# Optimization experiments

Measured on AMD Instinct MI355X. Metric: run time of the kernel, lower is better.

Reference implementation:

```python
import jax, jax.numpy as jnp
import numpy as np

DIM = 512
NUM_HEADS = 16
WIN = (7, 7)
SIZE = WIN[0] * WIN[1]  # 49
B = 2048   # total windows
NW = 4     # windows per image (mask groups)


def _relative_position_index():
    coords_h = np.arange(WIN[0])
    coords_w = np.arange(WIN[1])
    coords = np.stack(np.meshgrid(coords_h, coords_w, indexing='ij'))  # [2,Wh,Ww]
    flat = coords.reshape(2, -1)                                       # [2,S]
    rel = flat[:, :, None] - flat[:, None, :]                          # [2,S,S]
    rel = rel.transpose(1, 2, 0)                                       # [S,S,2]
    rel[:, :, 0] += WIN[0] - 1
    rel[:, :, 1] += WIN[1] - 1
    rel[:, :, 0] *= 2 * WIN[1] - 1
    return rel.sum(-1).astype(np.int32)                                # [S,S]


def setup_inputs() -> dict:
    key = jax.random.key(0)
    ks = jax.random.split(key, 8)
    num_bias = (2 * WIN[0] - 1) * (2 * WIN[1] - 1)  # 169
    sd = 1.0 / np.sqrt(DIM)
    return {
        'x': jax.random.normal(ks[0], (B, SIZE, DIM), dtype=jnp.float32),
        'mask': jax.random.normal(ks[1], (NW, SIZE, SIZE), dtype=jnp.float32),
        'w_qkv': jax.random.normal(ks[2], (DIM, 3 * DIM), dtype=jnp.float32) * sd,
        'b_qkv': jnp.zeros((3 * DIM,), dtype=jnp.float32),
        'w_proj': jax.random.normal(ks[3], (DIM, DIM), dtype=jnp.float32) * sd,
        'b_proj': jnp.zeros((DIM,), dtype=jnp.float32),
        'bias_table': jax.random.normal(ks[4], (num_bias, NUM_HEADS), dtype=jnp.float32) * 0.02,
        'rel_idx': jnp.asarray(_relative_position_index()),
    }


def reference(x, mask, w_qkv, b_qkv, w_proj, b_proj, bias_table, rel_idx):
    b, s, c = x.shape
    h = NUM_HEADS
    hd = c // h
    scale = hd ** (-0.5)
    # qkv projection -> [3, B, H, S, hd]
    qkv = (x @ w_qkv + b_qkv).reshape(b, s, 3, h, hd).transpose(2, 0, 3, 1, 4)
    q, k, v = qkv[0] * scale, qkv[1], qkv[2]
    attn = jnp.einsum('bhqd,bhkd->bhqk', q, k)                 # [B,H,S,S]
    # gathered relative position bias -> [H,S,S]
    bias = bias_table[rel_idx.reshape(-1)].reshape(s, s, h).transpose(2, 0, 1)
    attn = attn + bias[None]
    nw = mask.shape[0]
    attn = attn.reshape(b // nw, nw, h, s, s) + mask[None, :, None]
    attn = jax.nn.softmax(attn.reshape(b, h, s, s), axis=-1)
    out = jnp.einsum('bhqk,bhkd->bhqd', attn, v)               # [B,H,S,hd]
    out = out.transpose(0, 2, 1, 3).reshape(b, s, c)
    return out @ w_proj + b_proj
```

## Files before the change

### kernel.cpp

```cpp
#include <hip/hip_runtime.h>
#include <hip/hip_bf16.h>
#include <stdint.h>

typedef float  floatx4 __attribute__((ext_vector_type(4)));
typedef short  short8  __attribute__((ext_vector_type(8)));
typedef unsigned short u16;

#define DIM 512
#define NH 16
#define HD 32
#define WS 49
#define NBW 2048
#define NWIN 4
#define M_TOTAL (NBW*WS)
#define N_QKV (3*DIM)

__device__ __forceinline__ u16 f2bf(float f) {
    uint32_t u = __float_as_uint(f);
    u += 0x7FFFu + ((u >> 16) & 1u);
    return (u16)(u >> 16);
}

__device__ __forceinline__ void load_lds16(const u16* g, u16* l) {
    __builtin_amdgcn_global_load_lds(
        (const __attribute__((address_space(1))) unsigned int*)g,
        (__attribute__((address_space(3))) unsigned int*)l, 16, 0, 0);
}

__global__ void cast_x_kernel(const float* __restrict__ in, u16* __restrict__ out, int n4) {
    int i = blockIdx.x * blockDim.x + threadIdx.x;
    if (i >= n4) return;
    const float4 v = ((const float4*)in)[i];
    ushort4 o;
    o.x = f2bf(v.x); o.y = f2bf(v.y); o.z = f2bf(v.z); o.w = f2bf(v.w);
    ((ushort4*)out)[i] = o;
}

__global__ void transpose_cast_kernel(const float* __restrict__ in, u16* __restrict__ out,
                                      int N, int total) {
    int idx = blockIdx.x * blockDim.x + threadIdx.x;
    if (idx >= total) return;
    int k = idx & (DIM - 1);
    int n = idx >> 9;
    out[idx] = f2bf(in[k * N + n]);
}

__global__ void build_comb_kernel(const float* __restrict__ bias_table, const int* __restrict__ rel_idx,
                                  const float* __restrict__ mask, float* __restrict__ comb) {
    int idx = blockIdx.x * blockDim.x + threadIdx.x;
    if (idx >= NWIN * NH * 64 * 64) return;
    int c = idx & 3, jj = (idx >> 2) & 15, i = (idx >> 6) & 63, h = (idx >> 12) & 15, g = idx >> 16;
    int j = c * 16 + jj;
    float v = -1e30f;
    if (i < WS && j < WS)
        v = bias_table[rel_idx[i * WS + j] * NH + h] + mask[(g * WS + i) * WS + j];
    comb[idx] = v;
}

template<bool OUT_BF16>
__global__ __launch_bounds__(256, 2) void gemm_bt_kernel(
    const u16* __restrict__ A, const u16* __restrict__ Bt,
    const float* __restrict__ bias, void* __restrict__ out, int N, int K)
{
    __shared__ __align__(16) u16 sA[128 * 32];
    __shared__ __align__(16) u16 sB[128 * 32];
    const int tid  = threadIdx.x;
    const int lane = tid & 63;
    const int wave = tid >> 6;
    const long m0 = (long)blockIdx.y * 128;
    const long n0 = (long)blockIdx.x * 128;
    const int rr = lane & 15;
    const int qk = (lane >> 4) * 8;
    const int wm = (wave >> 1) * 64;
    const int wn = (wave & 1) * 64;

    floatx4 acc[4][4];
    const floatx4 z4 = {0.f, 0.f, 0.f, 0.f};
#pragma unroll
    for (int mi = 0; mi < 4; ++mi)
#pragma unroll
        for (int ni = 0; ni < 4; ++ni) acc[mi][ni] = z4;

    const int row0 = tid >> 2;
    const int kc0  = (tid & 3) * 8;
    const u16* gA0 = A  + (m0 + row0) * K + kc0;
    const u16* gA1 = A  + (m0 + row0 + 64) * K + kc0;
    const u16* gB0 = Bt + (n0 + row0) * K + kc0;
    const u16* gB1 = Bt + (n0 + row0 + 64) * K + kc0;
    u16* lA0 = sA + tid * 8;
    u16* lA1 = sA + (tid + 256) * 8;
    u16* lB0 = sB + tid * 8;
    u16* lB1 = sB + (tid + 256) * 8;

    for (int k0 = 0; k0 < K; k0 += 32) {
        load_lds16(gA0 + k0, lA0);
        load_lds16(gA1 + k0, lA1);
        load_lds16(gB0 + k0, lB0);
        load_lds16(gB1 + k0, lB1);
        __syncthreads();
        short8 af[4], bfr[4];
#pragma unroll
        for (int mi = 0; mi < 4; ++mi)
            af[mi] = *(const short8*)(sA + (wm + mi * 16 + rr) * 32 + qk);
#pragma unroll
        for (int ni = 0; ni < 4; ++ni)
            bfr[ni] = *(const short8*)(sB + (wn + ni * 16 + rr) * 32 + qk);
#pragma unroll
        for (int mi = 0; mi < 4; ++mi)
#pragma unroll
            for (int ni = 0; ni < 4; ++ni)
                acc[mi][ni] = __builtin_amdgcn_mfma_f32_16x16x32_bf16(af[mi], bfr[ni], acc[mi][ni], 0, 0, 0);
        __syncthreads();
    }

#pragma unroll
    for (int mi = 0; mi < 4; ++mi) {
#pragma unroll
        for (int r = 0; r < 4; ++r) {
            const long m = m0 + wm + mi * 16 + (lane >> 4) * 4 + r;
#pragma unroll
            for (int ni = 0; ni < 4; ++ni) {
                const long n = n0 + wn + ni * 16 + rr;
                float v = acc[mi][ni][r] + bias[n];
                if (OUT_BF16) ((u16*)out)[m * N + n] = f2bf(v);
                else          ((float*)out)[m * N + n] = v;
            }
        }
    }
}

__global__ __launch_bounds__(256, 4) void attn_kernel(
    const u16* __restrict__ qkv, const float* __restrict__ comb,
    u16* __restrict__ attn_out)
{
    const int w   = threadIdx.x >> 6;
    const int l   = threadIdx.x & 63;
    const int job = blockIdx.x * 4 + w;
    const int b    = job >> 5;
    const int h    = (job >> 1) & 15;
    const int half = job & 1;
    const int row0 = half * 32;
    const int rr = l & 15;
    const int q4 = l >> 4;
    const int qk = q4 * 8;

    __shared__ __align__(16) u16 p_s[4][32 * 64];
    u16* ps = p_s[w];

    const u16* qg = qkv + (long)b * WS * N_QKV + h * HD;
    const u16* kg = qg + DIM;
    const u16* vg = qg + 2 * DIM;

    const short8 z8 = {0, 0, 0, 0, 0, 0, 0, 0};
    const floatx4 z4 = {0.f, 0.f, 0.f, 0.f};

    short8 af[2], bfr[4];
#pragma unroll
    for (int mi = 0; mi < 2; ++mi) {
        const int row = row0 + mi * 16 + rr;
        af[mi] = (row < WS) ? *(const short8*)(qg + (long)row * N_QKV + qk) : z8;
    }
#pragma unroll
    for (int ni = 0; ni < 4; ++ni) {
        const int row = ni * 16 + rr;
        bfr[ni] = (row < WS) ? *(const short8*)(kg + (long)row * N_QKV + qk) : z8;
    }

    short8 vf[2][2];
#pragma unroll
    for (int kk = 0; kk < 2; ++kk)
#pragma unroll
        for (int ni = 0; ni < 2; ++ni) {
            short8 t = z8;
            const int d = 2 * rr + ni;
#pragma unroll
            for (int j = 0; j < 8; ++j) {
                const int s = kk * 32 + qk + j;
                if (s < WS) t[j] = (short)vg[(long)s * N_QKV + d];
            }
            vf[kk][ni] = t;
        }
    short8 vones;
#pragma unroll
    for (int j = 0; j < 8; ++j) vones[j] = (short)0x3F80;

    floatx4 sc[2][4];
#pragma unroll
    for (int mi = 0; mi < 2; ++mi)
#pragma unroll
        for (int ni = 0; ni < 4; ++ni)
            sc[mi][ni] = __builtin_amdgcn_mfma_f32_16x16x32_bf16(af[mi], bfr[ni], z4, 0, 0, 0);

    const float4* cb4 = (const float4*)comb + ((long)((b & (NWIN - 1)) * NH + h)) * 1024;
    const float scale = 0.17677669529663689f;
#pragma unroll
    for (int mi = 0; mi < 2; ++mi) {
#pragma unroll
        for (int r = 0; r < 4; ++r) {
            const int il = mi * 16 + q4 * 4 + r;
            const float4 cb = cb4[(row0 + il) * 16 + rr];
            float e0 = __expf(sc[mi][0][r] * scale + cb.x);
            float e1 = __expf(sc[mi][1][r] * scale + cb.y);
            float e2 = __expf(sc[mi][2][r] * scale + cb.z);
            float e3 = __expf(sc[mi][3][r] * scale + cb.w);
#pragma unroll
            for (int c = 0; c < 4; ++c) {
                const int col = c * 16 + rr;
                const int blk = (col >> 3) ^ (il & 7);
                const float ev = (c == 0) ? e0 : (c == 1) ? e1 : (c == 2) ? e2 : e3;
                ps[il * 64 + blk * 8 + (col & 7)] = f2bf(ev);
            }
        }
    }
    asm volatile("s_waitcnt lgkmcnt(0)" ::: "memory");

    floatx4 oacc[2][3];
#pragma unroll
    for (int mi = 0; mi < 2; ++mi) { oacc[mi][0] = z4; oacc[mi][1] = z4; oacc[mi][2] = z4; }
#pragma unroll
    for (int kk = 0; kk < 2; ++kk) {
        short8 pf[2];
#pragma unroll
        for (int mi = 0; mi < 2; ++mi) {
            const int i2 = mi * 16 + rr;
            pf[mi] = *(const short8*)(ps + i2 * 64 + (((4 * kk + q4) ^ (i2 & 7)) * 8));
        }
#pragma unroll
        for (int mi = 0; mi < 2; ++mi) {
            oacc[mi][0] = __builtin_amdgcn_mfma_f32_16x16x32_bf16(pf[mi], vf[kk][0], oacc[mi][0], 0, 0, 0);
            oacc[mi][1] = __builtin_amdgcn_mfma_f32_16x16x32_bf16(pf[mi], vf[kk][1], oacc[mi][1], 0, 0, 0);
            oacc[mi][2] = __builtin_amdgcn_mfma_f32_16x16x32_bf16(pf[mi], vones,     oacc[mi][2], 0, 0, 0);
        }
    }

#pragma unroll
    for (int mi = 0; mi < 2; ++mi) {
#pragma unroll
        for (int r = 0; r < 4; ++r) {
            const int ig = row0 + mi * 16 + q4 * 4 + r;
            if (ig < WS) {
                const float inv = 1.0f / oacc[mi][2][r];
                const uint32_t lo = f2bf(oacc[mi][0][r] * inv);
                const uint32_t hi = f2bf(oacc[mi][1][r] * inv);
                uint32_t* op = (uint32_t*)(attn_out + ((long)(b * WS + ig)) * DIM + h * HD);
                op[rr] = lo | (hi << 16);
            }
        }
    }
}

extern "C" void kernel_launch(void* const* d_in, const int* in_sizes, int n_in,
                              void* d_out, int out_size, void* d_ws, size_t ws_size,
                              hipStream_t stream)
{
    const float* x          = (const float*)d_in[0];
    const float* mask       = (const float*)d_in[1];
    const float* w_qkv      = (const float*)d_in[2];
    const float* b_qkv      = (const float*)d_in[3];
    const float* w_proj     = (const float*)d_in[4];
    const float* b_proj     = (const float*)d_in[5];
    const float* bias_table = (const float*)d_in[6];
    const int*   rel_idx    = (const int*)d_in[7];
    float* out = (float*)d_out;

    char* ws = (char*)d_ws;
    u16* x_bf   = (u16*)ws;  ws += (size_t)M_TOTAL * DIM * 2;
    u16* wqkvT  = (u16*)ws;  ws += (size_t)N_QKV * DIM * 2;
    u16* wprojT = (u16*)ws;  ws += (size_t)DIM * DIM * 2;
    float* comb = (float*)ws; ws += (size_t)NWIN * NH * 64 * 64 * 4;
    u16* qkv    = (u16*)ws;  ws += (size_t)M_TOTAL * N_QKV * 2;
    u16* attn_o = x_bf;

    const int n4 = M_TOTAL * DIM / 4;
    cast_x_kernel<<<(n4 + 255) / 256, 256, 0, stream>>>(x, x_bf, n4);
    transpose_cast_kernel<<<(N_QKV * DIM + 255) / 256, 256, 0, stream>>>(w_qkv, wqkvT, N_QKV, N_QKV * DIM);
    transpose_cast_kernel<<<(DIM * DIM + 255) / 256, 256, 0, stream>>>(w_proj, wprojT, DIM, DIM * DIM);
    build_comb_kernel<<<(NWIN * NH * 64 * 64 + 255) / 256, 256, 0, stream>>>(bias_table, rel_idx, mask, comb);

    gemm_bt_kernel<true><<<dim3(N_QKV / 128, M_TOTAL / 128), 256, 0, stream>>>(
        x_bf, wqkvT, b_qkv, qkv, N_QKV, DIM);

    attn_kernel<<<NBW * NH * 2 / 4, 256, 0, stream>>>(qkv, comb, attn_o);

    gemm_bt_kernel<false><<<dim3(DIM / 128, M_TOTAL / 128), 256, 0, stream>>>(
        attn_o, wprojT, b_proj, out, DIM, DIM);
}
```

Baseline: 856.7 us.

## Replace 128x128 GEMM with double-buffered 256x256 tile GEMM using XCD-aware block remap

Both projection GEMMs move to a 512-thread kernel with 256x256 output tiles and double-buffered LDS over 64-wide K steps. Global-to-LDS loads for the next stage are interleaved with MFMA phases, using explicit vmcnt waits, barriers and s_setprio. Blocks are remapped across the eight XCDs to improve L2 locality. This raises arithmetic intensity and overlaps memory with compute, at the cost of more registers (8x4 accumulators) and more LDS per block. M_TOTAL is 100352 = 392*256, so tiles divide evenly.

```diff
diff --git a/kernel.cpp b/kernel.cpp
--- a/kernel.cpp
+++ b/kernel.cpp
@@ -57,71 +57,134 @@
     comb[idx] = v;
 }
 
+#define STAGE_HALF(BASE, DST, Q, KH, KCOL)                                            \
+    do {                                                                              \
+        load_lds16((BASE) + (long)(s0 >> 2) * K + (KCOL) + (KH) * 32 + (s0 & 3) * 8,  \
+                   &DST[Q][KH][s0 * 8]);                                              \
+        load_lds16((BASE) + (long)(s1 >> 2) * K + (KCOL) + (KH) * 32 + (s1 & 3) * 8,  \
+                   &DST[Q][KH][s1 * 8]);                                              \
+    } while (0)
+
+#define LDA4(P, MG, KH)                                                               \
+    _Pragma("unroll")                                                                 \
+    for (int mi = 0; mi < 4; ++mi)                                                    \
+        af[mi] = *(const short8*)(&sA[P][KH][(wm + (MG) * 64 + mi * 16 + rr) * 32 + q4 * 8]);
+
+#define LDB4(P, KH)                                                                   \
+    _Pragma("unroll")                                                                 \
+    for (int ni = 0; ni < 4; ++ni)                                                    \
+        bf[ni] = *(const short8*)(&sB[P][KH][(wn + ni * 16 + rr) * 32 + q4 * 8]);
+
+#define MFMA16(MG)                                                                    \
+    _Pragma("unroll")                                                                 \
+    for (int mi = 0; mi < 4; ++mi)                                                    \
+        _Pragma("unroll")                                                             \
+        for (int ni = 0; ni < 4; ++ni)                                                \
+            acc[(MG) * 4 + mi][ni] = __builtin_amdgcn_mfma_f32_16x16x32_bf16(         \
+                af[mi], bf[ni], acc[(MG) * 4 + mi][ni], 0, 0, 0);
+
 template<bool OUT_BF16>
-__global__ __launch_bounds__(256, 2) void gemm_bt_kernel(
+__global__ __launch_bounds__(512, 2) void gemm256_kernel(
     const u16* __restrict__ A, const u16* __restrict__ Bt,
     const float* __restrict__ bias, void* __restrict__ out, int N, int K)
 {
-    __shared__ __align__(16) u16 sA[128 * 32];
-    __shared__ __align__(16) u16 sB[128 * 32];
+    __shared__ __align__(16) u16 sA[2][2][256 * 32];
+    __shared__ __align__(16) u16 sB[2][2][256 * 32];
+
     const int tid  = threadIdx.x;
     const int lane = tid & 63;
-    const int wave = tid >> 6;
-    const long m0 = (long)blockIdx.y * 128;
-    const long n0 = (long)blockIdx.x * 128;
-    const int rr = lane & 15;
-    const int qk = (lane >> 4) * 8;
-    const int wm = (wave >> 1) * 64;
-    const int wn = (wave & 1) * 64;
-
-    floatx4 acc[4][4];
+    const int w    = tid >> 6;
+    const int rr   = lane & 15;
+    const int q4   = lane >> 4;
+    const int wm   = (w >> 2) * 128;
+    const int wn   = (w & 3) * 64;
+
+    const int nwg = gridDim.x;
+    const int lid = (blockIdx.x & 7) * (nwg >> 3) + (blockIdx.x >> 3);
+    const int GX  = N >> 8;
+    const int bx  = lid % GX;
+    const int by  = lid / GX;
+    const long m0 = (long)by * 256;
+    const long n0 = (long)bx * 256;
+
+    const u16* Ab = A  + m0 * K;
+    const u16* Bb = Bt + n0 * K;
+
+    const int s0 = tid;
+    const int s1 = tid + 512;
+
+    floatx4 acc[8][4];
     const floatx4 z4 = {0.f, 0.f, 0.f, 0.f};
 #pragma unroll
-    for (int mi = 0; mi < 4; ++mi)
-#pragma unroll
-        for (int ni = 0; ni < 4; ++ni) acc[mi][ni] = z4;
-
-    const int row0 = tid >> 2;
-    const int kc0  = (tid & 3) * 8;
-    const u16* gA0 = A  + (m0 + row0) * K + kc0;
-    const u16* gA1 = A  + (m0 + row0 + 64) * K + kc0;
-    const u16* gB0 = Bt + (n0 + row0) * K + kc0;
-    const u16* gB1 = Bt + (n0 + row0 + 64) * K + kc0;
-    u16* lA0 = sA + tid * 8;
-    u16* lA1 = sA + (tid + 256) * 8;
-    u16* lB0 = sB + tid * 8;
-    u16* lB1 = sB + (tid + 256) * 8;
-
-    for (int k0 = 0; k0 < K; k0 += 32) {
-        load_lds16(gA0 + k0, lA0);
-        load_lds16(gA1 + k0, lA1);
-        load_lds16(gB0 + k0, lB0);
-        load_lds16(gB1 + k0, lB1);
-        __syncthreads();
-        short8 af[4], bfr[4];
-#pragma unroll
-        for (int mi = 0; mi < 4; ++mi)
-            af[mi] = *(const short8*)(sA + (wm + mi * 16 + rr) * 32 + qk);
-#pragma unroll
-        for (int ni = 0; ni < 4; ++ni)
-            bfr[ni] = *(const short8*)(sB + (wn + ni * 16 + rr) * 32 + qk);
-#pragma unroll
-        for (int mi = 0; mi < 4; ++mi)
-#pragma unroll
-            for (int ni = 0; ni < 4; ++ni)
-                acc[mi][ni] = __builtin_amdgcn_mfma_f32_16x16x32_bf16(af[mi], bfr[ni], acc[mi][ni], 0, 0, 0);
-        __syncthreads();
-    }
-
-#pragma unroll
-    for (int mi = 0; mi < 4; ++mi) {
-#pragma unroll
-        for (int r = 0; r < 4; ++r) {
-            const long m = m0 + wm + mi * 16 + (lane >> 4) * 4 + r;
-#pragma unroll
-            for (int ni = 0; ni < 4; ++ni) {
-                const long n = n0 + wn + ni * 16 + rr;
-                float v = acc[mi][ni][r] + bias[n];
+    for (int i = 0; i < 8; ++i)
+#pragma unroll
+        for (int j = 0; j < 4; ++j) acc[i][j] = z4;
+
+    const int nk = K >> 6;
+
+#pragma unroll
+    for (int kh = 0; kh < 2; ++kh) {
+        STAGE_HALF(Ab, sA, 0, kh, 0);
+        STAGE_HALF(Bb, sB, 0, kh, 0);
+    }
+    asm volatile("s_waitcnt vmcnt(4)" ::: "memory");
+    __builtin_amdgcn_s_barrier();
+
+    for (int it = 0; it < nk; ++it) {
+        const int  p  = it & 1, q = p ^ 1;
+        const int  kn = (it + 1) << 6;
+        const bool hn = (it + 1 < nk);
+        short8 af[4], bf[4];
+
+        if (hn) STAGE_HALF(Ab, sA, q, 0, kn);
+        LDB4(p, 0)
+        LDA4(p, 0, 0)
+        __builtin_amdgcn_s_barrier();
+        __builtin_amdgcn_s_setprio(1);
+        MFMA16(0)
+        __builtin_amdgcn_s_setprio(0);
+        __builtin_amdgcn_s_barrier();
+
+        if (hn) STAGE_HALF(Bb, sB, q, 0, kn);
+        LDA4(p, 1, 0)
+        __builtin_amdgcn_s_barrier();
+        __builtin_amdgcn_s_setprio(1);
+        MFMA16(1)
+        __builtin_amdgcn_s_setprio(0);
+        if (hn) { asm volatile("s_waitcnt vmcnt(4)" ::: "memory"); }
+        else    { asm volatile("s_waitcnt vmcnt(0)" ::: "memory"); }
+        __builtin_amdgcn_s_barrier();
+
+        if (hn) STAGE_HALF(Ab, sA, q, 1, kn);
+        LDB4(p, 1)
+        LDA4(p, 0, 1)
+        __builtin_amdgcn_s_barrier();
+        __builtin_amdgcn_s_setprio(1);
+        MFMA16(0)
+        __builtin_amdgcn_s_setprio(0);
+        __builtin_amdgcn_s_barrier();
+
+        if (hn) STAGE_HALF(Bb, sB, q, 1, kn);
+        LDA4(p, 1, 1)
+        __builtin_amdgcn_s_barrier();
+        __builtin_amdgcn_s_setprio(1);
+        MFMA16(1)
+        __builtin_amdgcn_s_setprio(0);
+        if (hn) { asm volatile("s_waitcnt vmcnt(4)" ::: "memory"); }
+        __builtin_amdgcn_s_barrier();
+    }
+
+#pragma unroll
+    for (int nf = 0; nf < 4; ++nf) {
+        const long n = n0 + wn + nf * 16 + rr;
+        const float bv = bias[n];
+#pragma unroll
+        for (int mf = 0; mf < 8; ++mf) {
+            const long mrow = m0 + wm + mf * 16 + q4 * 4;
+#pragma unroll
+            for (int r = 0; r < 4; ++r) {
+                const long m = mrow + r;
+                const float v = acc[mf][nf][r] + bv;
                 if (OUT_BF16) ((u16*)out)[m * N + n] = f2bf(v);
                 else          ((float*)out)[m * N + n] = v;
             }
@@ -277,11 +340,11 @@
     transpose_cast_kernel<<<(DIM * DIM + 255) / 256, 256, 0, stream>>>(w_proj, wprojT, DIM, DIM * DIM);
     build_comb_kernel<<<(NWIN * NH * 64 * 64 + 255) / 256, 256, 0, stream>>>(bias_table, rel_idx, mask, comb);
 
-    gemm_bt_kernel<true><<<dim3(N_QKV / 128, M_TOTAL / 128), 256, 0, stream>>>(
+    gemm256_kernel<true><<<dim3((M_TOTAL / 256) * (N_QKV / 256)), 512, 0, stream>>>(
         x_bf, wqkvT, b_qkv, qkv, N_QKV, DIM);
 
     attn_kernel<<<NBW * NH * 2 / 4, 256, 0, stream>>>(qkv, comb, attn_o);
 
-    gemm_bt_kernel<false><<<dim3(DIM / 128, M_TOTAL / 128), 256, 0, stream>>>(
+    gemm256_kernel<false><<<dim3((M_TOTAL / 256) * (DIM / 256)), 512, 0, stream>>>(
         attn_o, wprojT, b_proj, out, DIM, DIM);
 }
```

After: 939.4 us. 9.7% more time.
